# Kernel optimization log

Hardware: AMD Instinct MI355X
Metric: run time of the kernel (lower is better)

## Reference

```python
import jax, jax.numpy as jnp
import numpy as np

NUM_HEADS = 8
PROJ_DIM = 64
D_MODEL = 512


def setup_inputs() -> dict:
    key = jax.random.key(0)
    ks = jax.random.split(key, 10)
    B, SQ, SK = 4, 2048, 2048
    s_in = 1.0 / np.sqrt(D_MODEL)
    s_cat = 1.0 / np.sqrt(NUM_HEADS * PROJ_DIM)
    return {
        "query_seq": jax.random.normal(ks[0], (B, SQ, D_MODEL), jnp.float32),
        "store_seq": jax.random.normal(ks[1], (B, SK, D_MODEL), jnp.float32),
        "Wq": jax.random.normal(ks[2], (NUM_HEADS, D_MODEL, PROJ_DIM), jnp.float32) * s_in,
        "bq": jnp.zeros((NUM_HEADS, PROJ_DIM), jnp.float32),
        "Wk": jax.random.normal(ks[3], (D_MODEL, PROJ_DIM), jnp.float32) * s_in,
        "bk": jnp.zeros((PROJ_DIM,), jnp.float32),
        "Wv": jax.random.normal(ks[4], (D_MODEL, PROJ_DIM), jnp.float32) * s_in,
        "bv": jnp.zeros((PROJ_DIM,), jnp.float32),
        "Wo": jax.random.normal(ks[5], (NUM_HEADS * PROJ_DIM, PROJ_DIM), jnp.float32) * s_cat,
        "bo": jnp.zeros((PROJ_DIM,), jnp.float32),
    }


def reference(query_seq, store_seq, Wq, bq, Wk, bk, Wv, bv, Wo, bo):
    # Shared K/V projections: [B, Sk, P]
    k = store_seq @ Wk + bk
    v = store_seq @ Wv + bv
    # Per-head query projections, vectorized over heads: [B, H, Sq, P]
    q = jnp.einsum("bsd,hdp->bhsp", query_seq, Wq) + bq[None, :, None, :]
    scale = 1.0 / jnp.sqrt(jnp.asarray(PROJ_DIM, jnp.float32))
    # Scores against shared K: [B, H, Sq, Sk]
    scores = jnp.einsum("bhsp,btp->bhst", q, k) * scale
    attn = jax.nn.softmax(scores, axis=-1)
    # Attend over shared V: [B, H, Sq, P]
    o = jnp.einsum("bhst,btp->bhsp", attn, v)
    B, H, SQ, P = o.shape
    concat = jnp.transpose(o, (0, 2, 1, 3)).reshape(B, SQ, H * P)
    return concat @ Wo + bo
```

## Files before the change

### kernel.cpp

```cpp
#include <hip/hip_runtime.h>
#include <math.h>

#define BATCH   4
#define SEQQ    2048
#define SEQK    2048
#define DMODEL  512
#define NHEADS  8
#define PDIM    64

#define QSCALE  0.18033688f

typedef __attribute__((ext_vector_type(8))) short short8;
typedef __attribute__((ext_vector_type(4))) float f32x4;

__device__ __forceinline__ unsigned short f2bf(float x) {
    unsigned u = __builtin_bit_cast(unsigned, x);
    u += 0x7fffu + ((u >> 16) & 1u);
    return (unsigned short)(u >> 16);
}
__device__ __forceinline__ unsigned pack_bf16_rh(float lo, float hi) {
    unsigned ul = __builtin_bit_cast(unsigned, lo) + 0x8000u;
    unsigned uh = __builtin_bit_cast(unsigned, hi) + 0x8000u;
    return __builtin_amdgcn_perm(uh, ul, 0x07060302u);
}
__device__ __forceinline__ float bf2f_lo(unsigned w) {
    return __builtin_bit_cast(float, w << 16);
}
__device__ __forceinline__ float bf2f_hi(unsigned w) {
    return __builtin_bit_cast(float, w & 0xFFFF0000u);
}
__device__ __forceinline__ float exp2_raw(float x) {
    return __builtin_amdgcn_exp2f(x);
}
__device__ __forceinline__ void glds16(const void* g, void* l) {
    __builtin_amdgcn_global_load_lds(
        (const __attribute__((address_space(1))) void*)g,
        (__attribute__((address_space(3))) void*)l, 16, 0, 0);
}

__global__ __launch_bounds__(256) void convert_w_kernel(
    const float* __restrict__ Wq, const float* __restrict__ Wk,
    const float* __restrict__ Wv, const float* __restrict__ Wo,
    unsigned short* __restrict__ Wt)
{
    const int tid = threadIdx.x;
    const int mat = blockIdx.x;
    const float sc = (mat < 8) ? QSCALE : 1.0f;
    const float* src = (mat < 8) ? (Wq + (size_t)mat * 32768)
                     : (mat == 8) ? Wk : (mat == 9) ? Wv : Wo;
    __shared__ unsigned short T[64][72];
    for (int k0 = 0; k0 < 512; k0 += 64) {
#pragma unroll
        for (int it = 0; it < 4; ++it) {
            int flat = tid * 4 + 1024 * it;
            int k = flat >> 6, n = flat & 63;
            float4 v = *(const float4*)(src + (size_t)(k0 + k) * 64 + n);
            T[n + 0][k] = f2bf(v.x * sc);
            T[n + 1][k] = f2bf(v.y * sc);
            T[n + 2][k] = f2bf(v.z * sc);
            T[n + 3][k] = f2bf(v.w * sc);
        }
        __syncthreads();
        int n = tid >> 2, kk = (tid & 3) * 16;
        uint4 w0 = *(const uint4*)(&T[n][kk]);
        uint4 w1 = *(const uint4*)(&T[n][kk + 8]);
        *(uint4*)(Wt + (size_t)mat * 32768 + (size_t)n * 512 + k0 + kk) = w0;
        *(uint4*)(Wt + (size_t)mat * 32768 + (size_t)n * 512 + k0 + kk + 8) = w1;
        __syncthreads();
    }
}

__global__ __launch_bounds__(256, 4) void qkv_proj_kernel(
    const float* __restrict__ query, const float* __restrict__ store_,
    const unsigned short* __restrict__ Wt,
    const float* __restrict__ bq, const float* __restrict__ bk,
    const float* __restrict__ bv,
    unsigned short* __restrict__ Qbuf, unsigned short* __restrict__ Kbuf,
    unsigned short* __restrict__ Vtbuf)
{
    __shared__ unsigned short Xt[64 * 72];
    __shared__ unsigned short Wtile[128 * 64];

    const int slot = blockIdx.y;
    const int row0 = blockIdx.x * 64;
    const int b = row0 >> 11;
    const int s0 = row0 & 2047;
    const int matA = (slot < 4) ? 2 * slot : 8;

    const float* X = ((slot < 4) ? query : store_) + (size_t)row0 * 512;
    const unsigned short* WA = Wt + (size_t)matA * 32768;

    const int tid = threadIdx.x;
    const int wv = tid >> 6, lane = tid & 63;
    const int g = lane >> 4, c16 = lane & 15;
    const int c8 = c16 & 7;
    const int lrow = lane >> 3;
    const int lcol = ((lane & 7) ^ lrow) * 8;

    f32x4 z = {0.f, 0.f, 0.f, 0.f};
    f32x4 acc[8] = {z, z, z, z, z, z, z, z};

    const int xcol = (tid & 15) * 4;
    for (int k0 = 0; k0 < 512; k0 += 64) {
        float4 xr[4];
        int xrow[4];
#pragma unroll
        for (int it = 0; it < 4; ++it) {
            xrow[it] = (tid >> 4) + 16 * it;
            xr[it] = *(const float4*)(X + (size_t)xrow[it] * 512 + k0 + xcol);
        }
        __syncthreads();
#pragma unroll
        for (int j = 0; j < 4; ++j) {
            int rb = (4 * wv + j) * 8;
            glds16(WA + (size_t)(rb + lrow) * 512 + k0 + lcol, Wtile + rb * 64);
        }
#pragma unroll
        for (int it = 0; it < 4; ++it) {
            ushort4 o;
            o.x = f2bf(xr[it].x); o.y = f2bf(xr[it].y);
            o.z = f2bf(xr[it].z); o.w = f2bf(xr[it].w);
            *(ushort4*)(&Xt[xrow[it] * 72 + xcol]) = o;
        }
        __syncthreads();
#pragma unroll
        for (int ks = 0; ks < 2; ++ks) {
            short8 aX = *(const short8*)(&Xt[(16 * wv + c16) * 72 + 32 * ks + 8 * g]);
#pragma unroll
            for (int u = 0; u < 8; ++u) {
                short8 bW = *(const short8*)(Wtile + (16 * u + c16) * 64 + ((4 * ks + g) ^ c8) * 8);
                acc[u] = __builtin_amdgcn_mfma_f32_16x16x32_bf16(aX, bW, acc[u], 0, 0, 0);
            }
        }
    }

    if (slot < 4) {
#pragma unroll
        for (int m = 0; m < 2; ++m) {
            int head = 2 * slot + m;
            const float* bias = bq + head * 64;
            unsigned short* Y = Qbuf + ((size_t)(b * NHEADS + head) * SEQQ + s0) * PDIM;
#pragma unroll
            for (int uu = 0; uu < 4; ++uu) {
                float bb = QSCALE * bias[16 * uu + c16];
#pragma unroll
                for (int rr = 0; rr < 4; ++rr)
                    Y[(size_t)(16 * wv + 4 * g + rr) * PDIM + 16 * uu + c16] =
                        f2bf(acc[4 * m + uu][rr] + bb);
            }
        }
    } else {
        unsigned short* Yk = Kbuf + (size_t)row0 * PDIM;
#pragma unroll
        for (int uu = 0; uu < 4; ++uu) {
            float bb = bk[16 * uu + c16];
#pragma unroll
            for (int rr = 0; rr < 4; ++rr)
                Yk[(size_t)(16 * wv + 4 * g + rr) * PDIM + 16 * uu + c16] =
                    f2bf(acc[uu][rr] + bb);
        }
        __syncthreads();
#pragma unroll
        for (int uu = 0; uu < 4; ++uu) {
            float bb = bv[16 * uu + c16];
#pragma unroll
            for (int rr = 0; rr < 4; ++rr)
                Xt[(16 * uu + c16) * 72 + (16 * wv + 4 * g + rr)] =
                    f2bf(acc[4 + uu][rr] + bb);
        }
        __syncthreads();
        int p = tid >> 2, soff = (tid & 3) * 16;
        uint4 w0 = *(const uint4*)(&Xt[p * 72 + soff]);
        uint4 w1 = *(const uint4*)(&Xt[p * 72 + soff + 8]);
        unsigned short* dst = Vtbuf + (size_t)b * PDIM * SEQK + (size_t)p * SEQK + s0 + soff;
        *(uint4*)(dst) = w0;
        *(uint4*)(dst + 8) = w1;
    }
}

__global__ __launch_bounds__(256, 4) void attn_kernel(
    const unsigned short* __restrict__ Qbuf,
    const unsigned short* __restrict__ Kbuf,
    const unsigned short* __restrict__ Vtbuf,
    unsigned int* __restrict__ rawO,
    float* __restrict__ Lraw)
{
    __shared__ unsigned short smem[20480];
    unsigned short* Kb = smem;
    unsigned short* Vb = smem + 8192;
    unsigned short* Ps = smem + 16384;

    const int tid = threadIdx.x;
    const int wv = tid >> 6;
    const int lane = tid & 63;
    const int g = lane >> 4;
    const int c16 = lane & 15;
    const int c8 = c16 & 7;
    const int split = blockIdx.z & 1;
    const int b = blockIdx.z >> 1;
    const int h = blockIdx.y;
    const int qt = blockIdx.x;
    const int q0 = qt * 128;

    const int lrow = lane >> 3;
    const int lcol = ((lane & 7) ^ lrow) * 8;

    const unsigned short* Qp = Qbuf + ((size_t)(b * NHEADS + h) * SEQQ + q0) * PDIM;
#pragma unroll
    for (int j = 0; j < 4; ++j) {
        int rowblk = (4 * wv + j) * 8;
        glds16(Qp + (size_t)(rowblk + lrow) * PDIM + lcol, smem + rowblk * 64);
    }
    __syncthreads();

    short8 bQ[2][2];
#pragma unroll
    for (int y = 0; y < 2; ++y)
#pragma unroll
        for (int ks = 0; ks < 2; ++ks)
            bQ[y][ks] = *(const short8*)(smem + (32 * wv + 16 * y + c16) * 64 +
                                         ((4 * ks + g) ^ c8) * 8);
    __syncthreads();

    const unsigned short* Kp  = Kbuf  + (size_t)b * SEQK * PDIM + (size_t)split * 1024 * PDIM;
    const unsigned short* Vtp = Vtbuf + (size_t)b * PDIM * SEQK + split * 1024;

#pragma unroll
    for (int j = 0; j < 2; ++j) {
        int rb = (2 * wv + j) * 8;
        glds16(Kp + (size_t)(rb + lrow) * PDIM + lcol, Kb + rb * 64);
        glds16(Vtp + (size_t)(rb + lrow) * SEQK + lcol, Vb + rb * 64);
    }

    const short one_bf = (short)0x3F80;
    short8 vones = {one_bf, one_bf, one_bf, one_bf, one_bf, one_bf, one_bf, one_bf};

    f32x4 z = {0.f, 0.f, 0.f, 0.f};
    f32x4 oacc[2][4] = {{z, z, z, z}, {z, z, z, z}};
    f32x4 lacc[2] = {z, z};
    unsigned short* PsW = Ps + wv * 1024;

    for (int i = 0; i < 16; ++i) {
        __syncthreads();
        const unsigned short* Kc = Kb + (i & 1) * 4096;
        const unsigned short* Vc = Vb + (i & 1) * 4096;
        if (i < 15) {
            int t0 = (i + 1) * 64;
            unsigned short* Kn = Kb + ((i + 1) & 1) * 4096;
            unsigned short* Vn = Vb + ((i + 1) & 1) * 4096;
#pragma unroll
            for (int j = 0; j < 2; ++j) {
                int rb = (2 * wv + j) * 8;
                glds16(Kp + (size_t)(t0 + rb + lrow) * PDIM + lcol, Kn + rb * 64);
                glds16(Vtp + (size_t)(rb + lrow) * SEQK + t0 + lcol, Vn + rb * 64);
            }
        }

        f32x4 s0a[4] = {z, z, z, z};
        f32x4 s1a[4] = {z, z, z, z};
#pragma unroll
        for (int ks = 0; ks < 2; ++ks) {
#pragma unroll
            for (int t = 0; t < 4; ++t) {
                short8 aK = *(const short8*)(Kc + (16 * t + c16) * 64 + ((4 * ks + g) ^ c8) * 8);
                s0a[t] = __builtin_amdgcn_mfma_f32_16x16x32_bf16(aK, bQ[0][ks], s0a[t], 0, 0, 0);
                s1a[t] = __builtin_amdgcn_mfma_f32_16x16x32_bf16(aK, bQ[1][ks], s1a[t], 0, 0, 0);
            }
        }

        short8 aP[2][2];
#pragma unroll
        for (int y = 0; y < 2; ++y) {
            const f32x4* sc = y ? s1a : s0a;
#pragma unroll
            for (int t = 0; t < 4; ++t) {
                float p0 = exp2_raw(sc[t][0]);
                float p1 = exp2_raw(sc[t][1]);
                float p2 = exp2_raw(sc[t][2]);
                float p3 = exp2_raw(sc[t][3]);
                uint2 w2;
                w2.x = pack_bf16_rh(p0, p1);
                w2.y = pack_bf16_rh(p2, p3);
                int phys = (2 * t + (g >> 1)) ^ c8;
                *(uint2*)(PsW + c16 * 64 + phys * 8 + 4 * (g & 1)) = w2;
            }
#pragma unroll
            for (int ks = 0; ks < 2; ++ks)
                aP[y][ks] = *(const short8*)(PsW + c16 * 64 + ((4 * ks + g) ^ c8) * 8);
        }

#pragma unroll
        for (int ks = 0; ks < 2; ++ks) {
            lacc[0] = __builtin_amdgcn_mfma_f32_16x16x32_bf16(aP[0][ks], vones, lacc[0], 0, 0, 0);
            lacc[1] = __builtin_amdgcn_mfma_f32_16x16x32_bf16(aP[1][ks], vones, lacc[1], 0, 0, 0);
#pragma unroll
            for (int u = 0; u < 4; ++u) {
                short8 bV = *(const short8*)(Vc + (16 * u + c16) * 64 + ((4 * ks + g) ^ c8) * 8);
                oacc[0][u] = __builtin_amdgcn_mfma_f32_16x16x32_bf16(aP[0][ks], bV, oacc[0][u], 0, 0, 0);
                oacc[1][u] = __builtin_amdgcn_mfma_f32_16x16x32_bf16(aP[1][ks], bV, oacc[1][u], 0, 0, 0);
            }
        }
    }

    const int rawblk = ((b * NHEADS + h) * 16 + qt) * 2 + split;
    unsigned int* rb = rawO + (size_t)rawblk * 4096;
#pragma unroll
    for (int y = 0; y < 2; ++y) {
#pragma unroll
        for (int u = 0; u < 4; ++u) {
            int slot = (wv * 2 + y) * 4 + u;
            uint2 w2;
            w2.x = pack_bf16_rh(oacc[y][u][0], oacc[y][u][1]);
            w2.y = pack_bf16_rh(oacc[y][u][2], oacc[y][u][3]);
            *(uint2*)(rb + slot * 128 + lane * 2) = w2;
        }
        if (c16 == 0) {
#pragma unroll
            for (int r = 0; r < 4; ++r)
                Lraw[(size_t)rawblk * 128 + 32 * wv + 16 * y + 4 * g + r] = lacc[y][r];
        }
    }
}

__global__ __launch_bounds__(256) void out_proj_kernel(
    const unsigned int* __restrict__ rawO, const float* __restrict__ Lraw,
    const unsigned short* __restrict__ Wt, const float* __restrict__ bo,
    float* __restrict__ out)
{
    __shared__ unsigned short XtS[32 * 136];
    __shared__ unsigned short WtS[64 * 136];

    const int tid = threadIdx.x;
    const int wv = tid >> 6, lane = tid & 63;
    const int g = lane >> 4, c16 = lane & 15;
    const int row0 = blockIdx.x * 32;
    const int b = row0 >> 11;
    const int qt = (row0 & 2047) >> 7;
    const int off = row0 & 127;
    const unsigned short* W = Wt + (size_t)10 * 32768;

    const int sm = wv & 1;
    const int uh = wv >> 1;

    f32x4 z = {0.f, 0.f, 0.f, 0.f};
    f32x4 acc[2] = {z, z};

    for (int ch = 0; ch < 4; ++ch) {
        const int h0 = 2 * ch;
        uint4 wreg[4];
        int wrow[4], wkk[4];
#pragma unroll
        for (int it = 0; it < 4; ++it) {
            int flat = tid * 8 + 2048 * it;
            wrow[it] = flat >> 7; wkk[it] = flat & 127;
            int hh = wkk[it] >> 6;
            wreg[it] = *(const uint4*)(W + (size_t)wrow[it] * 512 + (h0 + hh) * 64 + (wkk[it] & 63));
        }
        unsigned short vv[2][2][4];
#pragma unroll
        for (int hh = 0; hh < 2; ++hh) {
            int h = h0 + hh;
            int rb0 = ((b * NHEADS + h) * 16 + qt) * 2;
            const unsigned int* p0 = rawO + (size_t)rb0 * 4096;
            const unsigned int* p1 = rawO + (size_t)(rb0 + 1) * 4096;
            const float* l0 = Lraw + (size_t)rb0 * 128;
            const float* l1 = Lraw + (size_t)(rb0 + 1) * 128;
#pragma unroll
            for (int sl = 0; sl < 2; ++sl) {
                int s_local = 2 * wv + sl;
                int m = s_local >> 2, u = s_local & 3;
                int sglob = ((off >> 4) + m) * 4 + u;
                uint2 a0 = *(const uint2*)(p0 + sglob * 128 + lane * 2);
                uint2 a1 = *(const uint2*)(p1 + sglob * 128 + lane * 2);
                float iv[4];
#pragma unroll
                for (int r = 0; r < 4; ++r) {
                    int q = off + 16 * m + 4 * g + r;
                    iv[r] = 1.0f / (l0[q] + l1[q]);
                }
                vv[hh][sl][0] = f2bf((bf2f_lo(a0.x) + bf2f_lo(a1.x)) * iv[0]);
                vv[hh][sl][1] = f2bf((bf2f_hi(a0.x) + bf2f_hi(a1.x)) * iv[1]);
                vv[hh][sl][2] = f2bf((bf2f_lo(a0.y) + bf2f_lo(a1.y)) * iv[2]);
                vv[hh][sl][3] = f2bf((bf2f_hi(a0.y) + bf2f_hi(a1.y)) * iv[3]);
            }
        }
        __syncthreads();
#pragma unroll
        for (int it = 0; it < 4; ++it)
            *(uint4*)(&WtS[wrow[it] * 136 + wkk[it]]) = wreg[it];
#pragma unroll
        for (int hh = 0; hh < 2; ++hh)
#pragma unroll
            for (int sl = 0; sl < 2; ++sl) {
                int s_local = 2 * wv + sl;
                int m = s_local >> 2, u = s_local & 3;
#pragma unroll
                for (int r = 0; r < 4; ++r)
                    XtS[(16 * m + 4 * g + r) * 136 + hh * 64 + 16 * u + c16] = vv[hh][sl][r];
            }
        __syncthreads();

#pragma unroll
        for (int hh = 0; hh < 2; ++hh)
#pragma unroll
            for (int ks = 0; ks < 2; ++ks) {
                short8 aX = *(const short8*)(&XtS[(16 * sm + c16) * 136 + hh * 64 + 32 * ks + 8 * g]);
#pragma unroll
                for (int uu = 0; uu < 2; ++uu) {
                    int u = 2 * uh + uu;
                    short8 bW = *(const short8*)(&WtS[(16 * u + c16) * 136 + hh * 64 + 32 * ks + 8 * g]);
                    acc[uu] = __builtin_amdgcn_mfma_f32_16x16x32_bf16(aX, bW, acc[uu], 0, 0, 0);
                }
            }
    }

#pragma unroll
    for (int uu = 0; uu < 2; ++uu) {
        int u = 2 * uh + uu;
        float bb = bo[16 * u + c16];
#pragma unroll
        for (int r = 0; r < 4; ++r)
            out[(size_t)(row0 + 16 * sm + 4 * g + r) * 64 + 16 * u + c16] = acc[uu][r] + bb;
    }
}

extern "C" void kernel_launch(void* const* d_in, const int* in_sizes, int n_in,
                              void* d_out, int out_size, void* d_ws, size_t ws_size,
                              hipStream_t stream) {
    const float* query = (const float*)d_in[0];
    const float* store_ = (const float*)d_in[1];
    const float* Wq    = (const float*)d_in[2];
    const float* bq    = (const float*)d_in[3];
    const float* Wk    = (const float*)d_in[4];
    const float* bk    = (const float*)d_in[5];
    const float* Wv    = (const float*)d_in[6];
    const float* bv    = (const float*)d_in[7];
    const float* Wo    = (const float*)d_in[8];
    const float* bo    = (const float*)d_in[9];
    float* out = (float*)d_out;

    unsigned short* Wt   = (unsigned short*)d_ws;
    unsigned short* Qbuf = Wt + (size_t)11 * 32768;
    unsigned short* Kbuf = Qbuf + (size_t)BATCH * NHEADS * SEQQ * PDIM;
    unsigned short* Vtbuf = Kbuf + (size_t)BATCH * SEQK * PDIM;
    unsigned int* rawO   = (unsigned int*)(Vtbuf + (size_t)BATCH * PDIM * SEQK);
    float* Lraw          = (float*)(rawO + (size_t)1024 * 4096);

    convert_w_kernel<<<11, 256, 0, stream>>>(Wq, Wk, Wv, Wo, Wt);

    dim3 gProj((BATCH * SEQQ) / 64, 5);
    qkv_proj_kernel<<<gProj, 256, 0, stream>>>(query, store_, Wt, bq, bk, bv,
                                               Qbuf, Kbuf, Vtbuf);

    dim3 gAttn(SEQQ / 128, NHEADS, BATCH * 2);
    attn_kernel<<<gAttn, 256, 0, stream>>>(Qbuf, Kbuf, Vtbuf, rawO, Lraw);

    out_proj_kernel<<<(BATCH * SEQQ) / 32, 256, 0, stream>>>(rawO, Lraw, Wt, bo, out);
}
```

Measured before the change: 179.6 us.

## Retile QKV projection to four heads per block and widen conversion and out-proj chunks

Weight conversion is split across 88 blocks, one per 64-row slice, so it no longer runs on only 11 workgroups. The QKV projection now uses 32-row tiles and computes four Q heads per block, or K and V together, over 3 slots instead of 5. Each loaded query tile is therefore reused for twice as many heads, which reduces redundant fp32 activation reads and conversions. The output projection processes four heads per chunk in two iterations, halving the barriers. The larger LDS footprint may lower occupancy.

```diff
diff --git a/kernel.cpp b/kernel.cpp
--- a/kernel.cpp
+++ b/kernel.cpp
@@ -44,30 +44,28 @@
     unsigned short* __restrict__ Wt)
 {
     const int tid = threadIdx.x;
-    const int mat = blockIdx.x;
+    const int mat = blockIdx.x >> 3;
+    const int k0 = (blockIdx.x & 7) << 6;
     const float sc = (mat < 8) ? QSCALE : 1.0f;
     const float* src = (mat < 8) ? (Wq + (size_t)mat * 32768)
                      : (mat == 8) ? Wk : (mat == 9) ? Wv : Wo;
     __shared__ unsigned short T[64][72];
-    for (int k0 = 0; k0 < 512; k0 += 64) {
-#pragma unroll
-        for (int it = 0; it < 4; ++it) {
-            int flat = tid * 4 + 1024 * it;
-            int k = flat >> 6, n = flat & 63;
-            float4 v = *(const float4*)(src + (size_t)(k0 + k) * 64 + n);
-            T[n + 0][k] = f2bf(v.x * sc);
-            T[n + 1][k] = f2bf(v.y * sc);
-            T[n + 2][k] = f2bf(v.z * sc);
-            T[n + 3][k] = f2bf(v.w * sc);
-        }
-        __syncthreads();
-        int n = tid >> 2, kk = (tid & 3) * 16;
-        uint4 w0 = *(const uint4*)(&T[n][kk]);
-        uint4 w1 = *(const uint4*)(&T[n][kk + 8]);
-        *(uint4*)(Wt + (size_t)mat * 32768 + (size_t)n * 512 + k0 + kk) = w0;
-        *(uint4*)(Wt + (size_t)mat * 32768 + (size_t)n * 512 + k0 + kk + 8) = w1;
-        __syncthreads();
-    }
+#pragma unroll
+    for (int it = 0; it < 4; ++it) {
+        int flat = tid * 4 + 1024 * it;
+        int k = flat >> 6, n = flat & 63;
+        float4 v = *(const float4*)(src + (size_t)(k0 + k) * 64 + n);
+        T[n + 0][k] = f2bf(v.x * sc);
+        T[n + 1][k] = f2bf(v.y * sc);
+        T[n + 2][k] = f2bf(v.z * sc);
+        T[n + 3][k] = f2bf(v.w * sc);
+    }
+    __syncthreads();
+    int n = tid >> 2, kk = (tid & 3) * 16;
+    uint4 w0 = *(const uint4*)(&T[n][kk]);
+    uint4 w1 = *(const uint4*)(&T[n][kk + 8]);
+    *(uint4*)(Wt + (size_t)mat * 32768 + (size_t)n * 512 + k0 + kk) = w0;
+    *(uint4*)(Wt + (size_t)mat * 32768 + (size_t)n * 512 + k0 + kk + 8) = w1;
 }
 
 __global__ __launch_bounds__(256, 4) void qkv_proj_kernel(
@@ -78,103 +76,112 @@
     unsigned short* __restrict__ Qbuf, unsigned short* __restrict__ Kbuf,
     unsigned short* __restrict__ Vtbuf)
 {
-    __shared__ unsigned short Xt[64 * 72];
-    __shared__ unsigned short Wtile[128 * 64];
+    __shared__ unsigned short Xt[2560];
+    __shared__ unsigned short Wtile[256 * 64];
 
     const int slot = blockIdx.y;
-    const int row0 = blockIdx.x * 64;
+    const int row0 = blockIdx.x * 32;
     const int b = row0 >> 11;
     const int s0 = row0 & 2047;
-    const int matA = (slot < 4) ? 2 * slot : 8;
-
-    const float* X = ((slot < 4) ? query : store_) + (size_t)row0 * 512;
-    const unsigned short* WA = Wt + (size_t)matA * 32768;
+
+    const float* X = ((slot < 2) ? query : store_) + (size_t)row0 * 512;
+    const unsigned short* Wbase = Wt + (size_t)(slot * 4) * 32768;
 
     const int tid = threadIdx.x;
     const int wv = tid >> 6, lane = tid & 63;
     const int g = lane >> 4, c16 = lane & 15;
     const int c8 = c16 & 7;
+    const int sm = wv & 1;
+    const int uh = wv >> 1;
     const int lrow = lane >> 3;
     const int lcol = ((lane & 7) ^ lrow) * 8;
 
     f32x4 z = {0.f, 0.f, 0.f, 0.f};
     f32x4 acc[8] = {z, z, z, z, z, z, z, z};
 
-    const int xcol = (tid & 15) * 4;
+    const int xrow = tid >> 3;
+    const int xcol = (tid & 7) * 8;
+    const int nwr = (slot < 2) ? 8 : 4;
+
     for (int k0 = 0; k0 < 512; k0 += 64) {
-        float4 xr[4];
-        int xrow[4];
-#pragma unroll
-        for (int it = 0; it < 4; ++it) {
-            xrow[it] = (tid >> 4) + 16 * it;
-            xr[it] = *(const float4*)(X + (size_t)xrow[it] * 512 + k0 + xcol);
-        }
-        __syncthreads();
-#pragma unroll
-        for (int j = 0; j < 4; ++j) {
-            int rb = (4 * wv + j) * 8;
-            glds16(WA + (size_t)(rb + lrow) * 512 + k0 + lcol, Wtile + rb * 64);
-        }
-#pragma unroll
-        for (int it = 0; it < 4; ++it) {
-            ushort4 o;
-            o.x = f2bf(xr[it].x); o.y = f2bf(xr[it].y);
-            o.z = f2bf(xr[it].z); o.w = f2bf(xr[it].w);
-            *(ushort4*)(&Xt[xrow[it] * 72 + xcol]) = o;
-        }
-        __syncthreads();
-#pragma unroll
-        for (int ks = 0; ks < 2; ++ks) {
-            short8 aX = *(const short8*)(&Xt[(16 * wv + c16) * 72 + 32 * ks + 8 * g]);
-#pragma unroll
-            for (int u = 0; u < 8; ++u) {
-                short8 bW = *(const short8*)(Wtile + (16 * u + c16) * 64 + ((4 * ks + g) ^ c8) * 8);
-                acc[u] = __builtin_amdgcn_mfma_f32_16x16x32_bf16(aX, bW, acc[u], 0, 0, 0);
-            }
-        }
-    }
-
-    if (slot < 4) {
-#pragma unroll
-        for (int m = 0; m < 2; ++m) {
-            int head = 2 * slot + m;
-            const float* bias = bq + head * 64;
+        float4 xa = *(const float4*)(X + (size_t)xrow * 512 + k0 + xcol);
+        float4 xb = *(const float4*)(X + (size_t)xrow * 512 + k0 + xcol + 4);
+        __syncthreads();
+        for (int j = 0; j < nwr; ++j) {
+            int rb = (nwr * wv + j) * 8;
+            glds16(Wbase + (size_t)(rb + lrow) * 512 + k0 + lcol, Wtile + rb * 64);
+        }
+        ushort4 o0, o1;
+        o0.x = f2bf(xa.x); o0.y = f2bf(xa.y); o0.z = f2bf(xa.z); o0.w = f2bf(xa.w);
+        o1.x = f2bf(xb.x); o1.y = f2bf(xb.y); o1.z = f2bf(xb.z); o1.w = f2bf(xb.w);
+        *(ushort4*)(&Xt[xrow * 72 + xcol]) = o0;
+        *(ushort4*)(&Xt[xrow * 72 + xcol + 4]) = o1;
+        __syncthreads();
+
+        if (slot < 2) {
+#pragma unroll
+            for (int ks = 0; ks < 2; ++ks) {
+                short8 aX = *(const short8*)(&Xt[(16 * sm + c16) * 72 + 32 * ks + 8 * g]);
+#pragma unroll
+                for (int uu = 0; uu < 8; ++uu) {
+                    int u = 8 * uh + uu;
+                    short8 bW = *(const short8*)(Wtile + (16 * u + c16) * 64 + ((4 * ks + g) ^ c8) * 8);
+                    acc[uu] = __builtin_amdgcn_mfma_f32_16x16x32_bf16(aX, bW, acc[uu], 0, 0, 0);
+                }
+            }
+        } else {
+#pragma unroll
+            for (int ks = 0; ks < 2; ++ks) {
+                short8 aX = *(const short8*)(&Xt[(16 * sm + c16) * 72 + 32 * ks + 8 * g]);
+#pragma unroll
+                for (int uu = 0; uu < 4; ++uu) {
+                    int u = 4 * uh + uu;
+                    short8 bW = *(const short8*)(Wtile + (16 * u + c16) * 64 + ((4 * ks + g) ^ c8) * 8);
+                    acc[uu] = __builtin_amdgcn_mfma_f32_16x16x32_bf16(aX, bW, acc[uu], 0, 0, 0);
+                }
+            }
+        }
+    }
+
+    if (slot < 2) {
+#pragma unroll
+        for (int uu = 0; uu < 8; ++uu) {
+            int u = 8 * uh + uu;
+            int head = 4 * slot + (u >> 2);
+            int pc = 16 * (u & 3) + c16;
+            float bb = QSCALE * bq[head * 64 + pc];
             unsigned short* Y = Qbuf + ((size_t)(b * NHEADS + head) * SEQQ + s0) * PDIM;
 #pragma unroll
+            for (int r = 0; r < 4; ++r)
+                Y[(size_t)(16 * sm + 4 * g + r) * PDIM + pc] = f2bf(acc[uu][r] + bb);
+        }
+    } else {
+        if (uh == 0) {
+            unsigned short* Yk = Kbuf + (size_t)row0 * PDIM;
+#pragma unroll
             for (int uu = 0; uu < 4; ++uu) {
-                float bb = QSCALE * bias[16 * uu + c16];
-#pragma unroll
-                for (int rr = 0; rr < 4; ++rr)
-                    Y[(size_t)(16 * wv + 4 * g + rr) * PDIM + 16 * uu + c16] =
-                        f2bf(acc[4 * m + uu][rr] + bb);
-            }
-        }
-    } else {
-        unsigned short* Yk = Kbuf + (size_t)row0 * PDIM;
-#pragma unroll
-        for (int uu = 0; uu < 4; ++uu) {
-            float bb = bk[16 * uu + c16];
-#pragma unroll
-            for (int rr = 0; rr < 4; ++rr)
-                Yk[(size_t)(16 * wv + 4 * g + rr) * PDIM + 16 * uu + c16] =
-                    f2bf(acc[uu][rr] + bb);
-        }
-        __syncthreads();
-#pragma unroll
-        for (int uu = 0; uu < 4; ++uu) {
-            float bb = bv[16 * uu + c16];
-#pragma unroll
-            for (int rr = 0; rr < 4; ++rr)
-                Xt[(16 * uu + c16) * 72 + (16 * wv + 4 * g + rr)] =
-                    f2bf(acc[4 + uu][rr] + bb);
-        }
-        __syncthreads();
-        int p = tid >> 2, soff = (tid & 3) * 16;
-        uint4 w0 = *(const uint4*)(&Xt[p * 72 + soff]);
-        uint4 w1 = *(const uint4*)(&Xt[p * 72 + soff + 8]);
-        unsigned short* dst = Vtbuf + (size_t)b * PDIM * SEQK + (size_t)p * SEQK + s0 + soff;
-        *(uint4*)(dst) = w0;
-        *(uint4*)(dst + 8) = w1;
+                float bb = bk[16 * uu + c16];
+#pragma unroll
+                for (int r = 0; r < 4; ++r)
+                    Yk[(size_t)(16 * sm + 4 * g + r) * PDIM + 16 * uu + c16] =
+                        f2bf(acc[uu][r] + bb);
+            }
+        }
+        __syncthreads();
+        if (uh == 1) {
+#pragma unroll
+            for (int uu = 0; uu < 4; ++uu) {
+                int p = 16 * uu + c16;
+                float bb = bv[p];
+#pragma unroll
+                for (int r = 0; r < 4; ++r)
+                    Xt[p * 40 + 16 * sm + 4 * g + r] = f2bf(acc[uu][r] + bb);
+            }
+        }
+        __syncthreads();
+        int p = tid >> 2, soff = (tid & 3) * 8;
+        uint4 w = *(const uint4*)(&Xt[p * 40 + soff]);
+        *(uint4*)(Vtbuf + (size_t)b * PDIM * SEQK + (size_t)p * SEQK + s0 + soff) = w;
     }
 }
 
@@ -327,8 +334,8 @@
     const unsigned short* __restrict__ Wt, const float* __restrict__ bo,
     float* __restrict__ out)
 {
-    __shared__ unsigned short XtS[32 * 136];
-    __shared__ unsigned short WtS[64 * 136];
+    __shared__ unsigned short XtS[32 * 264];
+    __shared__ unsigned short WtS[64 * 264];
 
     const int tid = threadIdx.x;
     const int wv = tid >> 6, lane = tid & 63;
@@ -345,20 +352,19 @@
     f32x4 z = {0.f, 0.f, 0.f, 0.f};
     f32x4 acc[2] = {z, z};
 
-    for (int ch = 0; ch < 4; ++ch) {
-        const int h0 = 2 * ch;
-        uint4 wreg[4];
-        int wrow[4], wkk[4];
-#pragma unroll
-        for (int it = 0; it < 4; ++it) {
+    for (int ch = 0; ch < 2; ++ch) {
+        const int h0 = 4 * ch;
+        uint4 wreg[8];
+        int wrow[8], wkk[8];
+#pragma unroll
+        for (int it = 0; it < 8; ++it) {
             int flat = tid * 8 + 2048 * it;
-            wrow[it] = flat >> 7; wkk[it] = flat & 127;
-            int hh = wkk[it] >> 6;
-            wreg[it] = *(const uint4*)(W + (size_t)wrow[it] * 512 + (h0 + hh) * 64 + (wkk[it] & 63));
-        }
-        unsigned short vv[2][2][4];
-#pragma unroll
-        for (int hh = 0; hh < 2; ++hh) {
+            wrow[it] = flat >> 8; wkk[it] = flat & 255;
+            wreg[it] = *(const uint4*)(W + (size_t)wrow[it] * 512 + h0 * 64 + wkk[it]);
+        }
+        unsigned short vv[4][2][4];
+#pragma unroll
+        for (int hh = 0; hh < 4; ++hh) {
             int h = h0 + hh;
             int rb0 = ((b * NHEADS + h) * 16 + qt) * 2;
             const unsigned int* p0 = rawO + (size_t)rb0 * 4096;
@@ -386,29 +392,29 @@
         }
         __syncthreads();
 #pragma unroll
-        for (int it = 0; it < 4; ++it)
-            *(uint4*)(&WtS[wrow[it] * 136 + wkk[it]]) = wreg[it];
-#pragma unroll
-        for (int hh = 0; hh < 2; ++hh)
+        for (int it = 0; it < 8; ++it)
+            *(uint4*)(&WtS[wrow[it] * 264 + wkk[it]]) = wreg[it];
+#pragma unroll
+        for (int hh = 0; hh < 4; ++hh)
 #pragma unroll
             for (int sl = 0; sl < 2; ++sl) {
                 int s_local = 2 * wv + sl;
                 int m = s_local >> 2, u = s_local & 3;
 #pragma unroll
                 for (int r = 0; r < 4; ++r)
-                    XtS[(16 * m + 4 * g + r) * 136 + hh * 64 + 16 * u + c16] = vv[hh][sl][r];
-            }
-        __syncthreads();
-
-#pragma unroll
-        for (int hh = 0; hh < 2; ++hh)
+                    XtS[(16 * m + 4 * g + r) * 264 + hh * 64 + 16 * u + c16] = vv[hh][sl][r];
+            }
+        __syncthreads();
+
+#pragma unroll
+        for (int hh = 0; hh < 4; ++hh)
 #pragma unroll
             for (int ks = 0; ks < 2; ++ks) {
-                short8 aX = *(const short8*)(&XtS[(16 * sm + c16) * 136 + hh * 64 + 32 * ks + 8 * g]);
+                short8 aX = *(const short8*)(&XtS[(16 * sm + c16) * 264 + hh * 64 + 32 * ks + 8 * g]);
 #pragma unroll
                 for (int uu = 0; uu < 2; ++uu) {
                     int u = 2 * uh + uu;
-                    short8 bW = *(const short8*)(&WtS[(16 * u + c16) * 136 + hh * 64 + 32 * ks + 8 * g]);
+                    short8 bW = *(const short8*)(&WtS[(16 * u + c16) * 264 + hh * 64 + 32 * ks + 8 * g]);
                     acc[uu] = __builtin_amdgcn_mfma_f32_16x16x32_bf16(aX, bW, acc[uu], 0, 0, 0);
                 }
             }
@@ -427,16 +433,16 @@
 extern "C" void kernel_launch(void* const* d_in, const int* in_sizes, int n_in,
                               void* d_out, int out_size, void* d_ws, size_t ws_size,
                               hipStream_t stream) {
-    const float* query = (const float*)d_in[0];
+    const float* query  = (const float*)d_in[0];
     const float* store_ = (const float*)d_in[1];
-    const float* Wq    = (const float*)d_in[2];
-    const float* bq    = (const float*)d_in[3];
-    const float* Wk    = (const float*)d_in[4];
-    const float* bk    = (const float*)d_in[5];
-    const float* Wv    = (const float*)d_in[6];
-    const float* bv    = (const float*)d_in[7];
-    const float* Wo    = (const float*)d_in[8];
-    const float* bo    = (const float*)d_in[9];
+    const float* Wq     = (const float*)d_in[2];
+    const float* bq     = (const float*)d_in[3];
+    const float* Wk     = (const float*)d_in[4];
+    const float* bk     = (const float*)d_in[5];
+    const float* Wv     = (const float*)d_in[6];
+    const float* bv     = (const float*)d_in[7];
+    const float* Wo     = (const float*)d_in[8];
+    const float* bo     = (const float*)d_in[9];
     float* out = (float*)d_out;
 
     unsigned short* Wt   = (unsigned short*)d_ws;
@@ -446,9 +452,9 @@
     unsigned int* rawO   = (unsigned int*)(Vtbuf + (size_t)BATCH * PDIM * SEQK);
     float* Lraw          = (float*)(rawO + (size_t)1024 * 4096);
 
-    convert_w_kernel<<<11, 256, 0, stream>>>(Wq, Wk, Wv, Wo, Wt);
-
-    dim3 gProj((BATCH * SEQQ) / 64, 5);
+    convert_w_kernel<<<88, 256, 0, stream>>>(Wq, Wk, Wv, Wo, Wt);
+
+    dim3 gProj((BATCH * SEQQ) / 32, 3);
     qkv_proj_kernel<<<gProj, 256, 0, stream>>>(query, store_, Wt, bq, bk, bv,
                                                Qbuf, Kbuf, Vtbuf);
 
```

Measured after the change: 166.9 us. 7.0% less time.
